# Optimization experiments

Hardware: AMD Instinct MI355X
Metric: run time of the kernel (lower is better)

The kernel has to match this reference:

```python
import jax, jax.numpy as jnp
import numpy as np

B, C, H, W, CR = 8, 256, 128, 128, 32


def setup_inputs() -> dict:
    key = jax.random.key(0)
    ks = jax.random.split(key, 5)
    s = 0.05  # weight scale ~ conv init
    return {
        "x": jax.random.normal(ks[0], (B, C, H, W), jnp.float32),
        "Wq": jax.random.normal(ks[1], (CR, C), jnp.float32) * s,
        "bq": jnp.zeros((CR,), jnp.float32),
        "Wk": jax.random.normal(ks[2], (CR, C), jnp.float32) * s,
        "bk": jnp.zeros((CR,), jnp.float32),
        "Wv": jax.random.normal(ks[3], (CR, C), jnp.float32) * s,
        "bv": jnp.zeros((CR,), jnp.float32),
        "Wz": jax.random.normal(ks[4], (C, CR), jnp.float32) * s,
        "bz": jnp.zeros((C,), jnp.float32),
    }


def _conv1x1(w, b, x):
    # 1x1 conv == per-pixel channel matmul
    return jnp.einsum('oc,bchw->bohw', w, x) + b[None, :, None, None]


def reference(x, Wq, bq, Wk, bk, Wv, bv, Wz, bz):
    h = x.shape[2]
    q = _conv1x1(Wq, bq, x)   # (B,Cr,H,W)
    k = _conv1x1(Wk, bk, x)
    v = _conv1x1(Wv, bv, x)
    # column (height-axis) energies, -inf on diagonal to avoid double-counting self
    neg_inf_diag = jnp.where(jnp.eye(h, dtype=bool), -jnp.inf, 0.0)  # (H,H)
    energy_H = jnp.einsum('bchw,bciw->bwhi', q, k) + neg_inf_diag   # (B,W,H,H)
    energy_H = energy_H.transpose(0, 2, 1, 3)                        # (B,H,W,H)
    # row (width-axis) energies
    energy_W = jnp.einsum('bchw,bchj->bhwj', q, k)                   # (B,H,W,W)
    attn = jax.nn.softmax(jnp.concatenate([energy_H, energy_W], axis=-1), axis=-1)
    out = jnp.einsum('bciw,bhwi->bchw', v, attn[..., :h])
    out = out + jnp.einsum('bchj,bhwj->bchw', v, attn[..., h:])
    out = _conv1x1(Wz, bz, out)
    return out + x  # with_residual=True
```

## Files before the change

kernel.cpp:

```cpp
#include <hip/hip_runtime.h>
#include <stdint.h>


typedef __attribute__((ext_vector_type(8))) short bf16x8;
typedef __attribute__((ext_vector_type(4))) float f32x4;
union frag_u { uint4 u4; bf16x8 h8; };

__device__ __forceinline__ float bf2f(uint32_t u) {
  union { uint32_t i; float f; } v; v.i = u << 16; return v.f;
}
__device__ __forceinline__ float bf2f_hi(uint32_t u) {
  union { uint32_t i; float f; } v; v.i = u & 0xffff0000u; return v.f;
}
__device__ __forceinline__ uint32_t f2bf(float f) {
  union { float f; uint32_t i; } v; v.f = f;
  return (v.i + 0x7fffu + ((v.i >> 16) & 1u)) >> 16;
}
__device__ __forceinline__ uint32_t packpair(float lo, float hi) {
  return f2bf(lo) | (f2bf(hi) << 16);
}
__device__ __forceinline__ void unpack8(uint4 a, float* f) {
  f[0] = bf2f(a.x); f[1] = bf2f_hi(a.x);
  f[2] = bf2f(a.y); f[3] = bf2f_hi(a.y);
  f[4] = bf2f(a.z); f[5] = bf2f_hi(a.z);
  f[6] = bf2f(a.w); f[7] = bf2f_hi(a.w);
}
__device__ __forceinline__ float ld_any(const void* p, int i, int isf32) {
  return isf32 ? ((const float*)p)[i] : bf2f(((const uint16_t*)p)[i]);
}

__global__ void detect_kernel(const uint16_t* __restrict__ x, int* __restrict__ flag) {
  __shared__ int bad;
  if (threadIdx.x == 0) bad = 0;
  __syncthreads();
  int hit = 0;
#pragma unroll
  for (int s = 0; s < 16; ++s) {
    uint32_t u = x[(threadIdx.x * 16 + s) * 2];
    uint32_t e = (u >> 7) & 0xffu;
    if (e == 0u || e == 255u) hit = 1;
  }
  if (hit) atomicAdd(&bad, 1);
  __syncthreads();
  if (threadIdx.x == 0) flag[0] = (bad > 0) ? 1 : 0;
}

__global__ void prep_kernel(
    const int* __restrict__ flag,
    const void* __restrict__ Wq, const void* __restrict__ bq,
    const void* __restrict__ Wk, const void* __restrict__ bk,
    const void* __restrict__ Wv, const void* __restrict__ bv,
    const void* __restrict__ Wz, const void* __restrict__ bz,
    float* __restrict__ wb, float* __restrict__ wzf,
    float* __restrict__ bzf, uint16_t* __restrict__ wbf)
{
  int isf32 = flag[0];
  int t = blockIdx.x * 256 + threadIdx.x;
  if (t < 24576) {
    int n = t >> 8, kk = t & 255;
    int z = n >> 5, o = n & 31;
    const void* W = (z == 0) ? Wq : (z == 1) ? Wk : Wv;
    wbf[t] = (uint16_t)f2bf(ld_any(W, o * 256 + kk, isf32));
  }
  if (t < 96) {
    int z = t >> 5, o = t & 31;
    const void* bb = (z == 0) ? bq : (z == 1) ? bk : bv;
    wb[t] = ld_any(bb, o, isf32);
  }
  if (t < 8192) wzf[t] = ld_any(Wz, t, isf32);
  if (t < 256)  bzf[t] = ld_any(bz, t, isf32);
}

__global__ __launch_bounds__(256) void qkv_mfma(
    const int* __restrict__ flag, const void* __restrict__ x,
    const uint16_t* __restrict__ wbf, const float* __restrict__ wb,
    uint16_t* __restrict__ qcol, uint16_t* __restrict__ kcol,
    uint16_t* __restrict__ vcol, uint16_t* __restrict__ qrow,
    uint16_t* __restrict__ krow, uint16_t* __restrict__ vrow)
{
  __shared__ __align__(16) uint16_t Xs[128 * 40];
  int isf32 = flag[0];
  int bx = blockIdx.x;
  int b = bx >> 7, hrow = bx & 127;
  int t = threadIdx.x;
  int wv = t >> 6, L = t & 63, quad = L >> 4, l15 = L & 15;

  f32x4 acc[2][6];
#pragma unroll
  for (int mi = 0; mi < 2; ++mi)
#pragma unroll
    for (int nt = 0; nt < 6; ++nt) {
      f32x4 z0 = {0.f, 0.f, 0.f, 0.f};
      acc[mi][nt] = z0;
    }

  for (int kc = 0; kc < 8; ++kc) {
    int k0 = kc * 32;
    __syncthreads();
    if (isf32) {
      const float* xp = (const float*)x + ((size_t)b << 22)
                      + (size_t)k0 * 16384 + hrow * 128;
#pragma unroll
      for (int r = 0; r < 16; ++r) {
        int idx = r * 256 + t, k = idx >> 7, m = idx & 127;
        Xs[m * 40 + k] = (uint16_t)f2bf(xp[(size_t)k * 16384 + m]);
      }
    } else {
      const uint16_t* xp = (const uint16_t*)x + ((size_t)b << 22)
                         + (size_t)k0 * 16384 + hrow * 128;
#pragma unroll
      for (int r = 0; r < 16; ++r) {
        int idx = r * 256 + t, k = idx >> 7, m = idx & 127;
        Xs[m * 40 + k] = xp[(size_t)k * 16384 + m];
      }
    }
    __syncthreads();

    bf16x8 af[2];
#pragma unroll
    for (int mi = 0; mi < 2; ++mi) {
      frag_u fu;
      fu.u4 = *(const uint4*)(Xs + ((wv * 2 + mi) * 16 + l15) * 40 + quad * 8);
      af[mi] = fu.h8;
    }
#pragma unroll
    for (int nt = 0; nt < 6; ++nt) {
      frag_u bu;
      bu.u4 = *(const uint4*)(wbf + (nt * 16 + l15) * 256 + k0 + quad * 8);
#pragma unroll
      for (int mi = 0; mi < 2; ++mi)
        acc[mi][nt] = __builtin_amdgcn_mfma_f32_16x16x32_bf16(af[mi], bu.h8, acc[mi][nt], 0, 0, 0);
    }
  }

#pragma unroll
  for (int nt = 0; nt < 6; ++nt) {
    int n = nt * 16 + l15;
    float bias = wb[n];
    int z = nt >> 1;
    int no = n & 31;
    uint16_t* colb = (z == 0) ? qcol : (z == 1) ? kcol : vcol;
    uint16_t* rowb = (z == 0) ? qrow : (z == 1) ? krow : vrow;
    size_t rowbase = (size_t)(b * 128 + hrow) * 4096;
#pragma unroll
    for (int mi = 0; mi < 2; ++mi) {
#pragma unroll
      for (int r = 0; r < 4; ++r) {
        int m = (wv * 2 + mi) * 16 + quad * 4 + r;
        uint16_t val = (uint16_t)f2bf(acc[mi][nt][r] + bias);
        rowb[rowbase + (size_t)m * 32 + no] = val;
        colb[(size_t)(b * 128 + m) * 4096 + hrow * 32 + no] = val;
      }
    }
  }
}

__global__ __launch_bounds__(256) void attn_kernel(
    const uint16_t* __restrict__ q, const uint16_t* __restrict__ k,
    const uint16_t* __restrict__ v, uint16_t* __restrict__ O,
    float* __restrict__ s, int iscol)
{
  __shared__ __align__(16) uint16_t P[128 * 136];
  __shared__ __align__(16) uint16_t vT[32 * 136];

  int cid = blockIdx.x, b = cid >> 7, loc = cid & 127;
  int tid = threadIdx.x;
  const uint16_t* qc = q + (size_t)cid * 4096;
  const uint16_t* kc = k + (size_t)cid * 4096;
  const uint16_t* vc = v + (size_t)cid * 4096;

  for (int idx = tid; idx < 4096; idx += 256)
    vT[(idx & 31) * 136 + (idx >> 5)] = vc[idx];

  int wv = tid >> 6, L = tid & 63, quad = L >> 4, l15 = L & 15;

  bf16x8 aq[2];
#pragma unroll
  for (int mi = 0; mi < 2; ++mi) {
    frag_u fu;
    fu.u4 = *(const uint4*)(qc + ((wv * 2 + mi) * 16 + l15) * 32 + quad * 8);
    aq[mi] = fu.h8;
  }
  for (int nt = 0; nt < 8; ++nt) {
    frag_u bu;
    bu.u4 = *(const uint4*)(kc + (nt * 16 + l15) * 32 + quad * 8);
    int col = nt * 16 + l15;
#pragma unroll
    for (int mi = 0; mi < 2; ++mi) {
      f32x4 z0 = {0.f, 0.f, 0.f, 0.f};
      f32x4 d = __builtin_amdgcn_mfma_f32_16x16x32_bf16(aq[mi], bu.h8, z0, 0, 0, 0);
      int row0 = (wv * 2 + mi) * 16 + quad * 4;
#pragma unroll
      for (int r = 0; r < 4; ++r) {
        float pe = __expf(d[r]);
        if (iscol && (row0 + r) == col) pe = 0.f;
        P[(row0 + r) * 136 + col] = (uint16_t)f2bf(pe);
      }
    }
  }
  __syncthreads();

  if (tid < 128) {
    float ss = 0.f;
    for (int j = 0; j < 128; ++j) ss += bf2f(P[tid * 136 + j]);
    size_t sbase = (size_t)b * 16384 + (iscol ? loc : loc * 128);
    s[sbase + (size_t)tid * (iscol ? 128 : 1)] = ss;
  }

  f32x4 acc[2][2];
#pragma unroll
  for (int mi = 0; mi < 2; ++mi)
#pragma unroll
    for (int ni = 0; ni < 2; ++ni) {
      f32x4 z0 = {0.f, 0.f, 0.f, 0.f};
      acc[mi][ni] = z0;
    }
#pragma unroll
  for (int kk = 0; kk < 4; ++kk) {
    bf16x8 ap[2], bv2[2];
#pragma unroll
    for (int mi = 0; mi < 2; ++mi) {
      frag_u fu;
      fu.u4 = *(const uint4*)(P + ((wv * 2 + mi) * 16 + l15) * 136 + kk * 32 + quad * 8);
      ap[mi] = fu.h8;
    }
#pragma unroll
    for (int ni = 0; ni < 2; ++ni) {
      frag_u fu;
      fu.u4 = *(const uint4*)(vT + (ni * 16 + l15) * 136 + kk * 32 + quad * 8);
      bv2[ni] = fu.h8;
    }
#pragma unroll
    for (int mi = 0; mi < 2; ++mi)
#pragma unroll
      for (int ni = 0; ni < 2; ++ni)
        acc[mi][ni] = __builtin_amdgcn_mfma_f32_16x16x32_bf16(ap[mi], bv2[ni], acc[mi][ni], 0, 0, 0);
  }

  size_t obase = (size_t)b * 524288 + (size_t)(iscol ? loc * 32 : loc * 4096);
  int orstride = iscol ? 4096 : 32;
#pragma unroll
  for (int mi = 0; mi < 2; ++mi)
#pragma unroll
    for (int ni = 0; ni < 2; ++ni) {
      int col = ni * 16 + l15;
#pragma unroll
      for (int r = 0; r < 4; ++r) {
        int row = (wv * 2 + mi) * 16 + quad * 4 + r;
        O[obase + (size_t)row * orstride + col] = (uint16_t)f2bf(acc[mi][ni][r]);
      }
    }
}

#define CSPLIT 4
__global__ __launch_bounds__(256) void combine_zres(
    const int* __restrict__ flag, const void* __restrict__ x,
    const uint16_t* __restrict__ Ocol, const uint16_t* __restrict__ Orow,
    const float* __restrict__ scol, const float* __restrict__ srow,
    const float* __restrict__ wzf, const float* __restrict__ bzf,
    void* __restrict__ out)
{
  int isf32 = flag[0];
  int bid = blockIdx.x;
  int cgrp = bid & (CSPLIT - 1);
  int pixblk = bid >> 2;
  int p = pixblk * 256 + threadIdx.x;
  int b = p >> 14;
  int rem = p & 16383;

  float inv = 1.0f / (scol[p] + srow[p]);
  float of[32];
  const uint4* c4 = (const uint4*)(Ocol + (size_t)p * 32);
  const uint4* r4 = (const uint4*)(Orow + (size_t)p * 32);
#pragma unroll
  for (int g = 0; g < 4; ++g) {
    float a[8], bb[8];
    unpack8(c4[g], a);
    unpack8(r4[g], bb);
#pragma unroll
    for (int j = 0; j < 8; ++j) of[g * 8 + j] = (a[j] + bb[j]) * inv;
  }

  int c0 = cgrp * (256 / CSPLIT);
  int c1 = c0 + (256 / CSPLIT);

  if (isf32) {
    const float* xp = (const float*)x + ((size_t)b << 22) + rem;
    float* op = (float*)out + ((size_t)b << 22) + rem;
#pragma unroll 2
    for (int c = c0; c < c1; ++c) {
      const float* wc = wzf + c * 32;
      float xv = xp[(size_t)c << 14];
      float a0 = 0.f, a1 = 0.f, a2 = 0.f, a3 = 0.f;
#pragma unroll
      for (int r = 0; r < 8; ++r) {
        a0 += wc[r]      * of[r];
        a1 += wc[8 + r]  * of[8 + r];
        a2 += wc[16 + r] * of[16 + r];
        a3 += wc[24 + r] * of[24 + r];
      }
      op[(size_t)c << 14] = bzf[c] + (a0 + a1) + (a2 + a3) + xv;
    }
  } else {
    const uint16_t* xp = (const uint16_t*)x + ((size_t)b << 22) + rem;
    uint16_t* op = (uint16_t*)out + ((size_t)b << 22) + rem;
#pragma unroll 2
    for (int c = c0; c < c1; ++c) {
      const float* wc = wzf + c * 32;
      float xv = bf2f(xp[(size_t)c << 14]);
      float a0 = 0.f, a1 = 0.f, a2 = 0.f, a3 = 0.f;
#pragma unroll
      for (int r = 0; r < 8; ++r) {
        a0 += wc[r]      * of[r];
        a1 += wc[8 + r]  * of[8 + r];
        a2 += wc[16 + r] * of[16 + r];
        a3 += wc[24 + r] * of[24 + r];
      }
      float acci = bzf[c] + (a0 + a1) + (a2 + a3) + xv;
      op[(size_t)c << 14] = (uint16_t)f2bf(acci);
    }
  }
}

extern "C" void kernel_launch(void* const* d_in, const int* in_sizes, int n_in,
                              void* d_out, int out_size, void* d_ws, size_t ws_size,
                              hipStream_t stream) {
  char* ws = (char*)d_ws;
  int*   flag = (int*)(ws);
  float* wb   = (float*)(ws + 256);
  float* wzf  = (float*)(ws + 1024);
  float* bzf  = (float*)(ws + 33792);
  uint16_t* wbf = (uint16_t*)(ws + 34816);
  uint16_t* qt = (uint16_t*)(ws + 147456);
  uint16_t* kt = qt + 4194304;
  uint16_t* vt = kt + 4194304;
  uint16_t* qr = vt + 4194304;
  uint16_t* kr = qr + 4194304;
  uint16_t* vr = kr + 4194304;
  uint16_t* Ocol = (uint16_t*)(ws + 50479104);
  uint16_t* Orow = (uint16_t*)(ws + 58867712);
  float* scol = (float*)(ws + 67256320);
  float* srow = (float*)(ws + 67780608);

  detect_kernel<<<1, 256, 0, stream>>>((const uint16_t*)d_in[0], flag);
  prep_kernel<<<96, 256, 0, stream>>>(flag, d_in[1], d_in[2], d_in[3], d_in[4],
                                      d_in[5], d_in[6], d_in[7], d_in[8],
                                      wb, wzf, bzf, wbf);
  qkv_mfma<<<1024, 256, 0, stream>>>(flag, d_in[0], wbf, wb,
                                     qt, kt, vt, qr, kr, vr);
  attn_kernel<<<1024, 256, 0, stream>>>(qt, kt, vt, Ocol, scol, 1);
  attn_kernel<<<1024, 256, 0, stream>>>(qr, kr, vr, Orow, srow, 0);
  combine_zres<<<512 * CSPLIT, 256, 0, stream>>>(flag, d_in[0], Ocol, Orow,
                                                 scol, srow, wzf, bzf, d_out);
}
```

Before: 350.0 us.

## Swizzle shared-memory layouts, parallelize row sums, and reorder combine block mapping

```diff
diff --git a/kernel.cpp b/kernel.cpp
--- a/kernel.cpp
+++ b/kernel.cpp
@@ -15,9 +15,6 @@
 __device__ __forceinline__ uint32_t f2bf(float f) {
   union { float f; uint32_t i; } v; v.f = f;
   return (v.i + 0x7fffu + ((v.i >> 16) & 1u)) >> 16;
-}
-__device__ __forceinline__ uint32_t packpair(float lo, float hi) {
-  return f2bf(lo) | (f2bf(hi) << 16);
 }
 __device__ __forceinline__ void unpack8(uint4 a, float* f) {
   f[0] = bf2f(a.x); f[1] = bf2f_hi(a.x);
@@ -28,6 +25,9 @@
 __device__ __forceinline__ float ld_any(const void* p, int i, int isf32) {
   return isf32 ? ((const float*)p)[i] : bf2f(((const uint16_t*)p)[i]);
 }
+
+#define XS_SWZ(m, k)  ((m) * 40 + ((k) ^ ((((m) >> 3) & 3) << 3)))
+#define P_SWZ(r, c)   ((r) * 128 + ((c) ^ (((r) & 7) << 3)))
 
 __global__ void detect_kernel(const uint16_t* __restrict__ x, int* __restrict__ flag) {
   __shared__ int bad;
@@ -103,7 +103,7 @@
 #pragma unroll
       for (int r = 0; r < 16; ++r) {
         int idx = r * 256 + t, k = idx >> 7, m = idx & 127;
-        Xs[m * 40 + k] = (uint16_t)f2bf(xp[(size_t)k * 16384 + m]);
+        Xs[XS_SWZ(m, k)] = (uint16_t)f2bf(xp[(size_t)k * 16384 + m]);
       }
     } else {
       const uint16_t* xp = (const uint16_t*)x + ((size_t)b << 22)
@@ -111,7 +111,7 @@
 #pragma unroll
       for (int r = 0; r < 16; ++r) {
         int idx = r * 256 + t, k = idx >> 7, m = idx & 127;
-        Xs[m * 40 + k] = xp[(size_t)k * 16384 + m];
+        Xs[XS_SWZ(m, k)] = xp[(size_t)k * 16384 + m];
       }
     }
     __syncthreads();
@@ -119,8 +119,9 @@
     bf16x8 af[2];
 #pragma unroll
     for (int mi = 0; mi < 2; ++mi) {
+      int row = (wv * 2 + mi) * 16 + l15;
       frag_u fu;
-      fu.u4 = *(const uint4*)(Xs + ((wv * 2 + mi) * 16 + l15) * 40 + quad * 8);
+      fu.u4 = *(const uint4*)(Xs + XS_SWZ(row, quad * 8));
       af[mi] = fu.h8;
     }
 #pragma unroll
@@ -155,13 +156,13 @@
   }
 }
 
-__global__ __launch_bounds__(256) void attn_kernel(
+__global__ __launch_bounds__(256, 4) void attn_kernel(
     const uint16_t* __restrict__ q, const uint16_t* __restrict__ k,
     const uint16_t* __restrict__ v, uint16_t* __restrict__ O,
     float* __restrict__ s, int iscol)
 {
-  __shared__ __align__(16) uint16_t P[128 * 136];
-  __shared__ __align__(16) uint16_t vT[32 * 136];
+  __shared__ __align__(16) uint16_t P[128 * 128];
+  __shared__ __align__(16) uint16_t vT[32 * 128];
 
   int cid = blockIdx.x, b = cid >> 7, loc = cid & 127;
   int tid = threadIdx.x;
@@ -169,8 +170,10 @@
   const uint16_t* kc = k + (size_t)cid * 4096;
   const uint16_t* vc = v + (size_t)cid * 4096;
 
-  for (int idx = tid; idx < 4096; idx += 256)
-    vT[(idx & 31) * 136 + (idx >> 5)] = vc[idx];
+  for (int idx = tid; idx < 4096; idx += 256) {
+    int ch = idx & 31, i = idx >> 5;
+    vT[P_SWZ(ch, i)] = vc[idx];
+  }
 
   int wv = tid >> 6, L = tid & 63, quad = L >> 4, l15 = L & 15;
 
@@ -194,17 +197,27 @@
       for (int r = 0; r < 4; ++r) {
         float pe = __expf(d[r]);
         if (iscol && (row0 + r) == col) pe = 0.f;
-        P[(row0 + r) * 136 + col] = (uint16_t)f2bf(pe);
+        P[P_SWZ(row0 + r, col)] = (uint16_t)f2bf(pe);
       }
     }
   }
   __syncthreads();
 
-  if (tid < 128) {
+  {
+    int row = tid >> 1, hh = tid & 1;
     float ss = 0.f;
-    for (int j = 0; j < 128; ++j) ss += bf2f(P[tid * 136 + j]);
-    size_t sbase = (size_t)b * 16384 + (iscol ? loc : loc * 128);
-    s[sbase + (size_t)tid * (iscol ? 128 : 1)] = ss;
+    const uint2* pr = (const uint2*)(P + row * 128 + hh * 64);
+#pragma unroll 4
+    for (int j = 0; j < 16; ++j) {
+      uint2 u = pr[j];
+      ss += bf2f(u.x); ss += bf2f_hi(u.x);
+      ss += bf2f(u.y); ss += bf2f_hi(u.y);
+    }
+    ss += __shfl_xor(ss, 1);
+    if (hh == 0) {
+      size_t sbase = (size_t)b * 16384 + (iscol ? loc : loc * 128);
+      s[sbase + (size_t)row * (iscol ? 128 : 1)] = ss;
+    }
   }
 
   f32x4 acc[2][2];
@@ -220,14 +233,16 @@
     bf16x8 ap[2], bv2[2];
 #pragma unroll
     for (int mi = 0; mi < 2; ++mi) {
+      int row = (wv * 2 + mi) * 16 + l15;
       frag_u fu;
-      fu.u4 = *(const uint4*)(P + ((wv * 2 + mi) * 16 + l15) * 136 + kk * 32 + quad * 8);
+      fu.u4 = *(const uint4*)(P + P_SWZ(row, kk * 32 + quad * 8));
       ap[mi] = fu.h8;
     }
 #pragma unroll
     for (int ni = 0; ni < 2; ++ni) {
+      int ch = ni * 16 + l15;
       frag_u fu;
-      fu.u4 = *(const uint4*)(vT + (ni * 16 + l15) * 136 + kk * 32 + quad * 8);
+      fu.u4 = *(const uint4*)(vT + P_SWZ(ch, kk * 32 + quad * 8));
       bv2[ni] = fu.h8;
     }
 #pragma unroll
@@ -262,8 +277,8 @@
 {
   int isf32 = flag[0];
   int bid = blockIdx.x;
-  int cgrp = bid & (CSPLIT - 1);
-  int pixblk = bid >> 2;
+  int pixblk = bid & 511;
+  int cgrp = bid >> 9;
   int p = pixblk * 256 + threadIdx.x;
   int b = p >> 14;
   int rem = p & 16383;
```

New measurement: 345.1 us. About the same (-1.4%).
